# Optimization experiments

Measured on AMD Instinct MI355X. Metric: run time of the kernel, lower is better.

Reference implementation:

```python
import jax, jax.numpy as jnp
import numpy as np

B, F, N, D, P = 32, 32, 36, 2048, 512  # batch, frames, objects, input dim, projected dim


def setup_inputs() -> dict:
    key = jax.random.key(0)
    ks = jax.random.split(key, 8)
    s = 1.0 / np.sqrt(D).astype(np.float32)  # torch nn.Linear default init range
    u = lambda k, shape: jax.random.uniform(k, shape, jnp.float32, -s, s)
    return {
        "object_variable": jax.random.normal(ks[0], (B, F, N, D), jnp.float32),
        "W_proj": u(ks[1], (D, P)), "b_proj": u(ks[2], (P,)),
        "W_sigma": u(ks[3], (D, P)), "b_sigma": u(ks[4], (P,)),
        "W_psi": u(ks[5], (D, P)), "b_psi": u(ks[6], (P,)),
        "W_r": u(ks[7], (D, P)),  # bias=False
    }


def reference(object_variable, W_proj, b_proj, W_sigma, b_sigma, W_psi, b_psi, W_r):
    # Dropouts are identity in eval mode.
    x = object_variable                                   # [B,F,N,D]
    r_feat = x @ W_proj + b_proj                          # [B,F,N,P]
    sig = x @ W_sigma + b_sigma                           # [B,F,N,P]
    psi = x @ W_psi + b_psi                               # [B,F,N,P]
    a_coeff = jnp.einsum('bfnp,bfmp->bfnm', sig, psi)     # [B,F,N,N] unscaled QK^T
    a_hat = jax.nn.softmax(a_coeff, axis=-1)
    r_hat = jnp.einsum('bfnm,bfmp->bfnp', a_hat, x @ W_r) # AV matmul
    return (r_feat, r_hat)
```

## Files before the change

kernel.cpp:

```cpp
#include <hip/hip_runtime.h>
#include <hip/hip_fp16.h>
#include <stdint.h>

typedef _Float16 half2v __attribute__((ext_vector_type(2)));
typedef _Float16 half4v __attribute__((ext_vector_type(4)));
typedef _Float16 half8v __attribute__((ext_vector_type(8)));
typedef float    float4v __attribute__((ext_vector_type(4)));

#define KDIM 2048
#define PDIM 512
#define MROWS 36864
#define NOBJ 36
#define NTOT 2048
#define KT   32

__device__ __forceinline__ void gload_lds16(const void* g, void* l) {
    using gptr_t = const __attribute__((address_space(1))) unsigned int*;
    using lptr_t = __attribute__((address_space(3))) unsigned int*;
    __builtin_amdgcn_global_load_lds((gptr_t)(uintptr_t)g,
                                     (lptr_t)(uint32_t)(uintptr_t)l,
                                     16, 0, 0);
}

__global__ __launch_bounds__(256)
void cvt_x_kernel(const float* __restrict__ x, _Float16* __restrict__ xh) {
    const size_t i = ((size_t)blockIdx.x * 256 + threadIdx.x) * 8;
    float4v a = *(const float4v*)&x[i];
    float4v b = *(const float4v*)&x[i + 4];
    half8v h;
    h[0] = (_Float16)a[0]; h[1] = (_Float16)a[1];
    h[2] = (_Float16)a[2]; h[3] = (_Float16)a[3];
    h[4] = (_Float16)b[0]; h[5] = (_Float16)b[1];
    h[6] = (_Float16)b[2]; h[7] = (_Float16)b[3];
    *(half8v*)&xh[i] = h;
}

__global__ __launch_bounds__(256)
void cvt_w_kernel(const float* __restrict__ Wp, const float* __restrict__ Ws,
                  const float* __restrict__ Wq, const float* __restrict__ Wr,
                  _Float16* __restrict__ wt) {
    const int bid = blockIdx.x;
    const int mat = bid >> 10;
    const int t   = bid & 1023;
    const int kt  = t >> 4;
    const int pt  = t & 15;
    const float* W = (mat == 0) ? Wp : (mat == 1) ? Ws : (mat == 2) ? Wq : Wr;

    __shared__ float tile[32][33];
    const int tx = threadIdx.x & 31;
    const int ty = threadIdx.x >> 5;
    #pragma unroll
    for (int r = 0; r < 4; ++r) {
        const int k = kt * 32 + ty + r * 8;
        tile[ty + r * 8][tx] = W[(size_t)k * PDIM + pt * 32 + tx];
    }
    __syncthreads();
    #pragma unroll
    for (int r = 0; r < 4; ++r) {
        const int p = pt * 32 + ty + r * 8;
        const int n = mat * PDIM + p;
        wt[(size_t)n * KDIM + kt * 32 + tx] = (_Float16)tile[tx][ty + r * 8];
    }
}

#define BARRIER() __builtin_amdgcn_s_barrier()

#define STAGE_AH(b_, kt_, h_) do {                                            \
    const _Float16* g_ = pA + (size_t)(kt_) * 64 + (size_t)(h_) * 262144;     \
    char* l_ = (char*)sA + (b_) * 32768 + (h_) * 16384 + tid * 16;            \
    gload_lds16(g_, l_);                                                      \
    gload_lds16(g_ + 131072, l_ + 8192);                                      \
} while (0)

#define STAGE_BH(b_, kt_, h_) do {                                            \
    const _Float16* g_ = pB + (size_t)(kt_) * 64 + (size_t)(h_) * 262144;     \
    char* l_ = (char*)sB + (b_) * 32768 + (h_) * 16384 + tid * 16;            \
    gload_lds16(g_, l_);                                                      \
    gload_lds16(g_ + 131072, l_ + 8192);                                      \
} while (0)

#define LOAD_AF(b_, qm_) do {                                                 \
    const char* ba_ = (const char*)sA + (b_) * 32768 + wrbase;                \
    _Pragma("unroll")                                                         \
    for (int mi = 0; mi < 4; ++mi) {                                          \
        const int ro_ = ((qm_) * 64 + mi * 16 + r15) * 128;                   \
        af[mi][0] = *(const half8v*)(ba_ + ro_ + ck0);                        \
        af[mi][1] = *(const half8v*)(ba_ + ro_ + ck1);                        \
    }                                                                         \
} while (0)

#define LOAD_BF(b_, qn_, dst_) do {                                           \
    const char* bb_ = (const char*)sB + (b_) * 32768 + wcbase;                \
    _Pragma("unroll")                                                         \
    for (int ni = 0; ni < 2; ++ni) {                                          \
        const int ro_ = (rB0 + (qn_) * 32 + ni * 16 + r15) * 128;             \
        dst_[ni][0] = *(const half8v*)(bb_ + ro_ + ck0);                      \
        dst_[ni][1] = *(const half8v*)(bb_ + ro_ + ck1);                      \
    }                                                                         \
} while (0)

#define MFMA16(mb_, nb_, bf_) do {                                            \
    _Pragma("unroll")                                                         \
    for (int mi = 0; mi < 4; ++mi)                                            \
        _Pragma("unroll")                                                     \
        for (int ni = 0; ni < 2; ++ni) {                                      \
            acc[(mb_) + mi][(nb_) + ni] = __builtin_amdgcn_mfma_f32_16x16x32_f16( \
                af[mi][0], bf_[ni][0], acc[(mb_) + mi][(nb_) + ni], 0, 0, 0); \
            acc[(mb_) + mi][(nb_) + ni] = __builtin_amdgcn_mfma_f32_16x16x32_f16( \
                af[mi][1], bf_[ni][1], acc[(mb_) + mi][(nb_) + ni], 0, 0, 0); \
        }                                                                     \
} while (0)

#define ITER(t_, b_) do {                                                     \
    if ((t_) + 1 < KT) { STAGE_AH((b_) ^ 1, (t_) + 1, 0);                     \
                         STAGE_AH((b_) ^ 1, (t_) + 1, 1); }                   \
    LOAD_BF(b_, 0, b0); LOAD_BF(b_, 1, b1); LOAD_AF(b_, 0);                   \
    __builtin_amdgcn_s_setprio(1);                                            \
    MFMA16(0, 0, b0); MFMA16(0, 2, b1);                                       \
    __builtin_amdgcn_s_setprio(0);                                            \
    __builtin_amdgcn_sched_barrier(0);     \
    BARRIER();                                                                \
    if ((t_) + 2 < KT) { STAGE_BH(b_, (t_) + 2, 0);                           \
                         STAGE_BH(b_, (t_) + 2, 1); }                         \
    LOAD_AF(b_, 1);                                                           \
    __builtin_amdgcn_s_setprio(1);                                            \
    MFMA16(4, 0, b0); MFMA16(4, 2, b1);                                       \
    __builtin_amdgcn_s_setprio(0);                                            \
    if ((t_) + 2 < KT)      { asm volatile("s_waitcnt vmcnt(4)" ::: "memory"); } \
    else if ((t_) + 1 < KT) { asm volatile("s_waitcnt vmcnt(0)" ::: "memory"); } \
    BARRIER();                                                                \
} while (0)

__global__ __launch_bounds__(512, 2)
void proj_gemm(const _Float16* __restrict__ A, const _Float16* __restrict__ Bt,
               float* __restrict__ rfeat, _Float16* __restrict__ sg,
               _Float16* __restrict__ ph, _Float16* __restrict__ vh,
               const float* __restrict__ bp, const float* __restrict__ bs,
               const float* __restrict__ bq) {
    __shared__ _Float16 sA[2][2][8192];
    __shared__ _Float16 sB[2][2][8192];

    const int tid  = threadIdx.x;
    const int lane = tid & 63;
    const int wid  = tid >> 6;
    const int wr   = wid >> 2;
    const int wc   = wid & 3;
    const int r15  = lane & 15;
    const int k4   = lane >> 4;

    const int bid = blockIdx.x;
    const int swz = (bid & 7) * 144 + (bid >> 3);
    const int mt  = swz >> 3, nt = swz & 7;
    const int m0  = mt * 256, n0 = nt * 256;

    const int srow = tid >> 3;
    const int sk   = (tid & 7) ^ (srow & 7);
    const _Float16* pA = A  + (size_t)(m0 + srow) * KDIM + sk * 8;
    const _Float16* pB = Bt + (size_t)(n0 + srow) * KDIM + sk * 8;

    const int ck0 = ((k4)     ^ (r15 & 7)) * 16;
    const int ck1 = ((4 + k4) ^ (r15 & 7)) * 16;
    const int wrbase = wr * 16384;
    const int wcbase = (wc >> 1) * 16384;
    const int rB0    = (wc & 1) * 64;

    half8v af[4][2], b0[2][2], b1[2][2];
    float4v acc[8][4] = {};

    STAGE_AH(0, 0, 0); STAGE_AH(0, 0, 1);
    STAGE_BH(0, 0, 0); STAGE_BH(0, 0, 1);
    STAGE_BH(1, 1, 0); STAGE_BH(1, 1, 1);
    asm volatile("s_waitcnt vmcnt(4)" ::: "memory");
    BARRIER();

    for (int tt = 0; tt < KT; tt += 2) {
        ITER(tt, 0);
        ITER(tt + 1, 1);
    }

    const int seg = n0 >> 9;
    const int pn0 = (n0 & 511) + wc * 64;
    #pragma unroll
    for (int ni = 0; ni < 4; ++ni) {
        const int pcol = pn0 + ni * 16 + r15;
        float bias = 0.0f;
        if (seg == 0)      bias = bp[pcol];
        else if (seg == 1) bias = bs[pcol];
        else if (seg == 2) bias = bq[pcol];
        #pragma unroll
        for (int mi = 0; mi < 8; ++mi) {
            const int rb = m0 + wr * 128 + mi * 16 + k4 * 4;
            #pragma unroll
            for (int r = 0; r < 4; ++r) {
                const float val = acc[mi][ni][r] + bias;
                const size_t off = (size_t)(rb + r) * PDIM + pcol;
                if (seg == 0)      rfeat[off] = val;
                else if (seg == 1) sg[off] = (_Float16)val;
                else if (seg == 2) ph[off] = (_Float16)val;
                else               vh[off] = (_Float16)val;
            }
        }
    }
}

__global__ __launch_bounds__(256, 2)
void attn_kernel(const _Float16* __restrict__ sg, const _Float16* __restrict__ ph,
                 const _Float16* __restrict__ vh, float* __restrict__ rhat) {
    __shared__ _Float16 ss[NOBJ * 520];
    __shared__ _Float16 ps[NOBJ * 520];
    __shared__ float    Ls[NOBJ * 37];

    const int tid = threadIdx.x;
    const size_t base = (size_t)blockIdx.x * (NOBJ * PDIM);

    for (int c = tid; c < (NOBJ * PDIM / 8); c += 256) {
        const int row = c >> 6;
        const int col = (c & 63) * 8;
        *(half8v*)&ss[row * 520 + col] = *(const half8v*)&sg[base + row * PDIM + col];
        *(half8v*)&ps[row * 520 + col] = *(const half8v*)&ph[base + row * PDIM + col];
    }
    __syncthreads();

    if (tid < 144) {
        const int i0 = (tid / 12) * 3;
        const int j0 = (tid % 12) * 3;
        float accv[3][3] = {};
        for (int p = 0; p < PDIM; p += 8) {
            half8v si[3], pj[3];
            #pragma unroll
            for (int ii = 0; ii < 3; ++ii) si[ii] = *(const half8v*)&ss[(i0 + ii) * 520 + p];
            #pragma unroll
            for (int jj = 0; jj < 3; ++jj) pj[jj] = *(const half8v*)&ps[(j0 + jj) * 520 + p];
            #pragma unroll
            for (int ii = 0; ii < 3; ++ii)
                #pragma unroll
                for (int jj = 0; jj < 3; ++jj) {
                    float t = accv[ii][jj];
                    #pragma unroll
                    for (int q = 0; q < 4; ++q) {
                        half2v x2; x2[0] = si[ii][2 * q]; x2[1] = si[ii][2 * q + 1];
                        half2v y2; y2[0] = pj[jj][2 * q]; y2[1] = pj[jj][2 * q + 1];
                        t = __builtin_amdgcn_fdot2(x2, y2, t, false);
                    }
                    accv[ii][jj] = t;
                }
        }
        #pragma unroll
        for (int ii = 0; ii < 3; ++ii)
            #pragma unroll
            for (int jj = 0; jj < 3; ++jj)
                Ls[(i0 + ii) * 37 + (j0 + jj)] = accv[ii][jj];
    }
    __syncthreads();

    if (tid < NOBJ) {
        float mx = -1e30f;
        for (int j = 0; j < NOBJ; ++j) mx = fmaxf(mx, Ls[tid * 37 + j]);
        float sum = 0.0f;
        for (int j = 0; j < NOBJ; ++j) {
            float e = __expf(Ls[tid * 37 + j] - mx);
            sum += e;
            Ls[tid * 37 + j] = e;
        }
        const float inv = 1.0f / sum;
        for (int j = 0; j < NOBJ; ++j) Ls[tid * 37 + j] *= inv;
    }
    __syncthreads();

    const int p4 = (tid & 127) * 4;
    const int r0 = tid >> 7;
    float4v acc[18] = {};
    for (int j = 0; j < NOBJ; ++j) {
        half4v v4 = *(const half4v*)&vh[base + (size_t)j * PDIM + p4];
        float4v vf;
        vf[0] = (float)v4[0]; vf[1] = (float)v4[1];
        vf[2] = (float)v4[2]; vf[3] = (float)v4[3];
        #pragma unroll
        for (int m = 0; m < 18; ++m) {
            const float aw = Ls[(2 * m + r0) * 37 + j];
            acc[m] += aw * vf;
        }
    }
    #pragma unroll
    for (int m = 0; m < 18; ++m)
        *(float4v*)&rhat[base + (size_t)(2 * m + r0) * PDIM + p4] = acc[m];
}

extern "C" void kernel_launch(void* const* d_in, const int* in_sizes, int n_in,
                              void* d_out, int out_size, void* d_ws, size_t ws_size,
                              hipStream_t stream) {
    const float* x   = (const float*)d_in[0];
    const float* Wp  = (const float*)d_in[1];
    const float* bp  = (const float*)d_in[2];
    const float* Wsg = (const float*)d_in[3];
    const float* bsg = (const float*)d_in[4];
    const float* Wps = (const float*)d_in[5];
    const float* bps = (const float*)d_in[6];
    const float* Wr  = (const float*)d_in[7];
    float* out = (float*)d_out;

    char* ws = (char*)d_ws;
    _Float16* xh = (_Float16*)(ws);
    _Float16* wt = (_Float16*)(ws + 150994944UL);
    _Float16* sg = (_Float16*)(ws + 159383552UL);
    _Float16* ph = (_Float16*)(ws + 197132288UL);
    _Float16* vh = (_Float16*)(ws + 234881024UL);

    cvt_x_kernel<<<36864, 256, 0, stream>>>(x, xh);
    cvt_w_kernel<<<4096, 256, 0, stream>>>(Wp, Wsg, Wps, Wr, wt);
    proj_gemm<<<144 * 8, 512, 0, stream>>>(xh, wt, out, sg, ph, vh, bp, bsg, bps);
    attn_kernel<<<1024, 256, 0, stream>>>(sg, ph, vh, out + 18874368);
}
```

Measured before the change: 847.3 us.

## Fuse fp32-to-fp16 conversion of x into projection GEMM A-tile loading

Removes the separate conversion kernel that wrote a half-precision copy of x to workspace. The GEMM now loads fp32 x tiles into registers, converts them, and writes them to LDS with a swizzle. B staging moves to a triple buffer so each iteration needs only one barrier. The GEMM saves a full write and re-read of the converted activation, but it now reads fp32 data through registers. Occupancy drops to one block per CU, which raises register and LDS pressure.

```diff
diff --git a/kernel.cpp b/kernel.cpp
--- a/kernel.cpp
+++ b/kernel.cpp
@@ -20,19 +20,6 @@
     __builtin_amdgcn_global_load_lds((gptr_t)(uintptr_t)g,
                                      (lptr_t)(uint32_t)(uintptr_t)l,
                                      16, 0, 0);
-}
-
-__global__ __launch_bounds__(256)
-void cvt_x_kernel(const float* __restrict__ x, _Float16* __restrict__ xh) {
-    const size_t i = ((size_t)blockIdx.x * 256 + threadIdx.x) * 8;
-    float4v a = *(const float4v*)&x[i];
-    float4v b = *(const float4v*)&x[i + 4];
-    half8v h;
-    h[0] = (_Float16)a[0]; h[1] = (_Float16)a[1];
-    h[2] = (_Float16)a[2]; h[3] = (_Float16)a[3];
-    h[4] = (_Float16)b[0]; h[5] = (_Float16)b[1];
-    h[6] = (_Float16)b[2]; h[7] = (_Float16)b[3];
-    *(half8v*)&xh[i] = h;
 }
 
 __global__ __launch_bounds__(256)
@@ -65,18 +52,33 @@
 
 #define BARRIER() __builtin_amdgcn_s_barrier()
 
-#define STAGE_AH(b_, kt_, h_) do {                                            \
-    const _Float16* g_ = pA + (size_t)(kt_) * 64 + (size_t)(h_) * 262144;     \
-    char* l_ = (char*)sA + (b_) * 32768 + (h_) * 16384 + tid * 16;            \
-    gload_lds16(g_, l_);                                                      \
-    gload_lds16(g_ + 131072, l_ + 8192);                                      \
-} while (0)
-
 #define STAGE_BH(b_, kt_, h_) do {                                            \
     const _Float16* g_ = pB + (size_t)(kt_) * 64 + (size_t)(h_) * 262144;     \
     char* l_ = (char*)sB + (b_) * 32768 + (h_) * 16384 + tid * 16;            \
     gload_lds16(g_, l_);                                                      \
     gload_lds16(g_ + 131072, l_ + 8192);                                      \
+} while (0)
+
+#define A_ISSUE(kt_) do {                                                     \
+    const float* g_ = pX + (size_t)(kt_) * 64;                                \
+    _Pragma("unroll")                                                         \
+    for (int r_ = 0; r_ < 4; ++r_) {                                          \
+        asr[2 * r_]     = *(const float4v*)(g_ + (size_t)r_ * 64 * KDIM);     \
+        asr[2 * r_ + 1] = *(const float4v*)(g_ + (size_t)r_ * 64 * KDIM + 4); \
+    }                                                                         \
+} while (0)
+
+#define A_WRITE(bdst_) do {                                                   \
+    char* l_ = (char*)sA + (bdst_) * 32768 + dsAoff;                          \
+    _Pragma("unroll")                                                         \
+    for (int r_ = 0; r_ < 4; ++r_) {                                          \
+        half8v h_;                                                            \
+        h_[0] = (_Float16)asr[2*r_][0]; h_[1] = (_Float16)asr[2*r_][1];       \
+        h_[2] = (_Float16)asr[2*r_][2]; h_[3] = (_Float16)asr[2*r_][3];       \
+        h_[4] = (_Float16)asr[2*r_+1][0]; h_[5] = (_Float16)asr[2*r_+1][1];   \
+        h_[6] = (_Float16)asr[2*r_+1][2]; h_[7] = (_Float16)asr[2*r_+1][3];   \
+        *(half8v*)(l_ + r_ * 8192) = h_;                                      \
+    }                                                                         \
 } while (0)
 
 #define LOAD_AF(b_, qm_) do {                                                 \
@@ -111,34 +113,35 @@
         }                                                                     \
 } while (0)
 
-#define ITER(t_, b_) do {                                                     \
-    if ((t_) + 1 < KT) { STAGE_AH((b_) ^ 1, (t_) + 1, 0);                     \
-                         STAGE_AH((b_) ^ 1, (t_) + 1, 1); }                   \
-    LOAD_BF(b_, 0, b0); LOAD_BF(b_, 1, b1); LOAD_AF(b_, 0);                   \
+#define ITER(t_, bA_, bB_, bB2_) do {                                         \
+    if ((t_) + 1 < KT) A_ISSUE((t_) + 1);                                     \
+    if ((t_) + 2 < KT) { STAGE_BH(bB2_, (t_) + 2, 0);                         \
+                         STAGE_BH(bB2_, (t_) + 2, 1); }                       \
+    __builtin_amdgcn_sched_barrier(0);    \
+    LOAD_BF(bB_, 0, b0); LOAD_BF(bB_, 1, b1); LOAD_AF(bA_, 0);                \
     __builtin_amdgcn_s_setprio(1);                                            \
     MFMA16(0, 0, b0); MFMA16(0, 2, b1);                                       \
     __builtin_amdgcn_s_setprio(0);                                            \
-    __builtin_amdgcn_sched_barrier(0);     \
-    BARRIER();                                                                \
-    if ((t_) + 2 < KT) { STAGE_BH(b_, (t_) + 2, 0);                           \
-                         STAGE_BH(b_, (t_) + 2, 1); }                         \
-    LOAD_AF(b_, 1);                                                           \
+    LOAD_AF(bA_, 1);                                                          \
     __builtin_amdgcn_s_setprio(1);                                            \
     MFMA16(4, 0, b0); MFMA16(4, 2, b1);                                       \
     __builtin_amdgcn_s_setprio(0);                                            \
-    if ((t_) + 2 < KT)      { asm volatile("s_waitcnt vmcnt(4)" ::: "memory"); } \
-    else if ((t_) + 1 < KT) { asm volatile("s_waitcnt vmcnt(0)" ::: "memory"); } \
+    if ((t_) + 2 < KT) { asm volatile("s_waitcnt vmcnt(4)" ::: "memory"); }   \
+    else               { asm volatile("s_waitcnt vmcnt(0)" ::: "memory"); }   \
+    if ((t_) + 1 < KT) A_WRITE((bA_) ^ 1);                                    \
+    asm volatile("s_waitcnt lgkmcnt(0)" ::: "memory");                        \
     BARRIER();                                                                \
-} while (0)
-
-__global__ __launch_bounds__(512, 2)
-void proj_gemm(const _Float16* __restrict__ A, const _Float16* __restrict__ Bt,
+    __builtin_amdgcn_sched_barrier(0);                                        \
+} while (0)
+
+__global__ __launch_bounds__(512, 1)
+void proj_gemm(const float* __restrict__ X, const _Float16* __restrict__ Bt,
                float* __restrict__ rfeat, _Float16* __restrict__ sg,
                _Float16* __restrict__ ph, _Float16* __restrict__ vh,
                const float* __restrict__ bp, const float* __restrict__ bs,
                const float* __restrict__ bq) {
-    __shared__ _Float16 sA[2][2][8192];
-    __shared__ _Float16 sB[2][2][8192];
+    __shared__ _Float16 sA[2 * 16384];
+    __shared__ _Float16 sB[3 * 16384];
 
     const int tid  = threadIdx.x;
     const int lane = tid & 63;
@@ -153,9 +156,13 @@
     const int mt  = swz >> 3, nt = swz & 7;
     const int m0  = mt * 256, n0 = nt * 256;
 
+    const int arow = wid * 8 + (lane >> 3);
+    const int ac   = lane & 7;
+    const float* pX = X + (size_t)(m0 + arow) * KDIM + ac * 8;
+    const int dsAoff = arow * 128 + ((ac ^ (lane >> 3)) << 4);
+
     const int srow = tid >> 3;
     const int sk   = (tid & 7) ^ (srow & 7);
-    const _Float16* pA = A  + (size_t)(m0 + srow) * KDIM + sk * 8;
     const _Float16* pB = Bt + (size_t)(n0 + srow) * KDIM + sk * 8;
 
     const int ck0 = ((k4)     ^ (r15 & 7)) * 16;
@@ -165,17 +172,24 @@
     const int rB0    = (wc & 1) * 64;
 
     half8v af[4][2], b0[2][2], b1[2][2];
+    float4v asr[8];
     float4v acc[8][4] = {};
 
-    STAGE_AH(0, 0, 0); STAGE_AH(0, 0, 1);
+    A_ISSUE(0);
     STAGE_BH(0, 0, 0); STAGE_BH(0, 0, 1);
     STAGE_BH(1, 1, 0); STAGE_BH(1, 1, 1);
-    asm volatile("s_waitcnt vmcnt(4)" ::: "memory");
+    A_WRITE(0);
+    asm volatile("s_waitcnt vmcnt(4) lgkmcnt(0)" ::: "memory");
     BARRIER();
-
-    for (int tt = 0; tt < KT; tt += 2) {
-        ITER(tt, 0);
-        ITER(tt + 1, 1);
+    __builtin_amdgcn_sched_barrier(0);
+
+    int bA = 0, bB = 0, bB2 = 2;
+    #pragma unroll 2
+    for (int t = 0; t < KT; ++t) {
+        ITER(t, bA, bB, bB2);
+        bA ^= 1;
+        bB  = (bB  == 2) ? 0 : bB  + 1;
+        bB2 = (bB2 == 2) ? 0 : bB2 + 1;
     }
 
     const int seg = n0 >> 9;
@@ -300,14 +314,12 @@
     float* out = (float*)d_out;
 
     char* ws = (char*)d_ws;
-    _Float16* xh = (_Float16*)(ws);
-    _Float16* wt = (_Float16*)(ws + 150994944UL);
-    _Float16* sg = (_Float16*)(ws + 159383552UL);
-    _Float16* ph = (_Float16*)(ws + 197132288UL);
-    _Float16* vh = (_Float16*)(ws + 234881024UL);
-
-    cvt_x_kernel<<<36864, 256, 0, stream>>>(x, xh);
+    _Float16* wt = (_Float16*)(ws);
+    _Float16* sg = (_Float16*)(ws + 8388608UL);
+    _Float16* ph = (_Float16*)(ws + 46137344UL);
+    _Float16* vh = (_Float16*)(ws + 83886080UL);
+
     cvt_w_kernel<<<4096, 256, 0, stream>>>(Wp, Wsg, Wps, Wr, wt);
-    proj_gemm<<<144 * 8, 512, 0, stream>>>(xh, wt, out, sg, ph, vh, bp, bsg, bps);
+    proj_gemm<<<144 * 8, 512, 0, stream>>>(x, wt, out, sg, ph, vh, bp, bsg, bps);
     attn_kernel<<<1024, 256, 0, stream>>>(sg, ph, vh, out + 18874368);
 }
```

New measurement: 870.3 us. 1.03x slower.
